# Kernel tuning notes

Hardware: AMD Instinct MI355X
Metric: run time of the kernel (lower is better)

The kernel has to match this reference:

```python
import jax, jax.numpy as jnp
import numpy as np

OUT_F, IN_F = 4096, 4096
WEIGHT_NUMEL = OUT_F * IN_F
NUM_CHUNKS, CHUNK_SIZE = 16384, 1024
D_ALPHA, HIDDEN = 64, 256
TOKENS = 256


def setup_inputs() -> dict:
    key = jax.random.key(0)
    ks = jax.random.split(key, 7)
    s = 0.05  # keep activations in a sane range
    return {
        "x": jax.random.normal(ks[0], (TOKENS, IN_F), jnp.float32),
        "codebook": jax.random.normal(ks[1], (NUM_CHUNKS, D_ALPHA), jnp.float32) * s,
        "w1": jax.random.normal(ks[2], (HIDDEN, D_ALPHA), jnp.float32) * s,
        "b1": jax.random.normal(ks[3], (HIDDEN,), jnp.float32) * s,
        "w2": jax.random.normal(ks[4], (CHUNK_SIZE, HIDDEN), jnp.float32) * s,
        "b2": jax.random.normal(ks[5], (CHUNK_SIZE,), jnp.float32) * s,
        "bias": jax.random.normal(ks[6], (OUT_F,), jnp.float32) * s,
    }


def reference(x, codebook, w1, b1, w2, b2, bias):
    # materialize_weight: alpha = codebook[start:start+num_chunks] (here: all rows)
    alpha = codebook[:NUM_CHUNKS]                                  # [num_chunks, d_alpha]
    # shared decoder psi: Linear -> GELU(exact) -> Linear (chunked loop == single GEMM)
    h = jax.nn.gelu(alpha @ w1.T + b1, approximate=False)          # [num_chunks, hidden]
    chunks = h @ w2.T + b2                                         # [num_chunks, chunk_size]
    w = chunks.reshape(-1)[:WEIGHT_NUMEL].reshape(OUT_F, IN_F)     # assemble weight
    # F.linear(x, w, b) = x @ w.T + b
    return x @ w.T + bias
```

## Files before the change

### kernel.cpp

```cpp
#include <hip/hip_runtime.h>
#include <math.h>

#define OUT_F      4096
#define IN_F       4096
#define NUM_CHUNKS 16384
#define CHUNK_SIZE 1024
#define D_ALPHA    64
#define HIDDEN     256
#define TOKENS     256

typedef __attribute__((ext_vector_type(8))) __bf16 bf16x8;
typedef __attribute__((ext_vector_type(4))) __bf16 bf16x4;
typedef __attribute__((ext_vector_type(4))) float f32x4;

__device__ __forceinline__ void gl2lds16(const void* g, void* l) {
    __builtin_amdgcn_global_load_lds(
        (const __attribute__((address_space(1))) void*)g,
        (__attribute__((address_space(3))) void*)l,
        16, 0, 0);
}

__global__ __launch_bounds__(256) void prep_kernel(
    const float* __restrict__ cb, const float* __restrict__ w1,
    const float* __restrict__ b1, const float* __restrict__ x,
    const float* __restrict__ b2, const float* __restrict__ w2,
    __bf16* __restrict__ H, __bf16* __restrict__ xb,
    float* __restrict__ xb2, __bf16* __restrict__ w2t) {
    __shared__ char smem[16384];
    const int b   = blockIdx.x;
    const int tid = threadIdx.x;

    if (b < 1024) {
        const int by = b >> 2;
        const int bx = b & 3;
        const int c0 = by * 64, h0 = bx * 64;
        __bf16* sA = (__bf16*)smem;
        __bf16* sB = (__bf16*)(smem + 8192);
        const float4* cb4 = reinterpret_cast<const float4*>(cb) + (size_t)by * 1024;
        const float4* w14 = reinterpret_cast<const float4*>(w1) + (size_t)bx * 1024;
#pragma unroll
        for (int q = 0; q < 4; ++q) {
            const int idx = q * 256 + tid;
            float4 va = cb4[idx];
            float4 vb = w14[idx];
            bf16x4 oa, ob;
            oa.x = (__bf16)va.x; oa.y = (__bf16)va.y; oa.z = (__bf16)va.z; oa.w = (__bf16)va.w;
            ob.x = (__bf16)vb.x; ob.y = (__bf16)vb.y; ob.z = (__bf16)vb.z; ob.w = (__bf16)vb.w;
            *reinterpret_cast<bf16x4*>(sA + idx * 4) = oa;
            *reinterpret_cast<bf16x4*>(sB + idx * 4) = ob;
        }
        __syncthreads();
        const int wave = tid >> 6, lane = tid & 63;
        const int wm = (wave & 1) * 32, wn = (wave >> 1) * 32;
        const int fr = lane & 15, fq = lane >> 4;
        f32x4 acc[2][2] = {};
        bf16x8 af[2][2], bv[2][2];
#pragma unroll
        for (int i = 0; i < 2; ++i)
#pragma unroll
            for (int u = 0; u < 2; ++u) {
                af[i][u] = *reinterpret_cast<const bf16x8*>(
                    sA + (wm + i * 16 + fr) * 64 + u * 32 + fq * 8);
                bv[i][u] = *reinterpret_cast<const bf16x8*>(
                    sB + (wn + i * 16 + fr) * 64 + u * 32 + fq * 8);
            }
#pragma unroll
        for (int u = 0; u < 2; ++u)
#pragma unroll
            for (int i = 0; i < 2; ++i)
#pragma unroll
                for (int j = 0; j < 2; ++j)
                    acc[i][j] = __builtin_amdgcn_mfma_f32_16x16x32_bf16(
                        af[i][u], bv[j][u], acc[i][j], 0, 0, 0);
#pragma unroll
        for (int j = 0; j < 2; ++j) {
            const int col = h0 + wn + j * 16 + fr;
            const float bb = b1[col];
#pragma unroll
            for (int i = 0; i < 2; ++i) {
                const int rbase = c0 + wm + i * 16 + fq * 4;
#pragma unroll
                for (int r = 0; r < 4; ++r) {
                    float v = acc[i][j][r] + bb;
                    float g = 0.5f * v * (1.0f + erff(v * 0.70710678118654752f));
                    H[(size_t)(rbase + r) * 256 + col] = (__bf16)g;
                }
            }
        }
    } else if (b < 1280) {
        float* ws_ = (float*)smem;
        const int t = b - 1024;
        const float4* xr  = reinterpret_cast<const float4*>(x + (size_t)t * IN_F);
        const float4* b24 = reinterpret_cast<const float4*>(b2);
        bf16x4* xb4 = reinterpret_cast<bf16x4*>(xb + (size_t)t * IN_F);
        float acc = 0.0f;
#pragma unroll
        for (int ii = 0; ii < 4; ++ii) {
            const int idx = ii * 256 + tid;
            float4 v = xr[idx];
            bf16x4 o;
            o.x = (__bf16)v.x; o.y = (__bf16)v.y; o.z = (__bf16)v.z; o.w = (__bf16)v.w;
            xb4[idx] = o;
            float4 bb = b24[idx & 255];
            acc += v.x * bb.x + v.y * bb.y + v.z * bb.z + v.w * bb.w;
        }
#pragma unroll
        for (int off = 32; off > 0; off >>= 1) acc += __shfl_down(acc, off, 64);
        if ((tid & 63) == 0) ws_[tid >> 6] = acc;
        __syncthreads();
        if (tid == 0) xb2[t] = ws_[0] + ws_[1] + ws_[2] + ws_[3];
    } else {
        float (*tile)[33] = (float (*)[33])smem;
        const int bb = b - 1280;
        const int h0 = (bb & 7) * 32;
        const int p0 = (bb >> 3) * 32;
        const int r = tid >> 5;
        const int c = tid & 31;
#pragma unroll
        for (int ii = 0; ii < 4; ++ii)
            tile[r + 8 * ii][c] = w2[(size_t)(p0 + r + 8 * ii) * HIDDEN + h0 + c];
        __syncthreads();
#pragma unroll
        for (int ii = 0; ii < 4; ++ii)
            w2t[(size_t)(h0 + r + 8 * ii) * CHUNK_SIZE + p0 + c] =
                (__bf16)tile[c][r + 8 * ii];
    }
}

template <int BK, int EPI>
__global__ __launch_bounds__(256) void gemm_bt64(
    const __bf16* __restrict__ A, const __bf16* __restrict__ B,
    const float* __restrict__ bias, const float* __restrict__ rowterm,
    void* __restrict__ Cv, int M, int N, int K) {
    __shared__ __bf16 sA[64 * BK];
    __shared__ __bf16 sB[64 * BK];
    const int tid = threadIdx.x;
    const int m0 = blockIdx.y * 64;
    const int n0 = blockIdx.x * 64;

    constexpr int NC = BK / 32;
    int rowc[NC], colc[NC];
#pragma unroll
    for (int c = 0; c < NC; ++c) {
        const int flat = c * 2048 + tid * 8;
        rowc[c] = flat / BK;
        colc[c] = flat % BK;
    }

    const int wave = tid >> 6, lane = tid & 63;
    const int wm = (wave & 1) * 32, wn = (wave >> 1) * 32;
    const int fr = lane & 15, fq = lane >> 4;

    f32x4 acc[2][2] = {};

    for (int k0 = 0; k0 < K; k0 += BK) {
#pragma unroll
        for (int c = 0; c < NC; ++c) {
            gl2lds16(A + (size_t)(m0 + rowc[c]) * K + k0 + colc[c],
                     sA + c * 2048 + tid * 8);
            gl2lds16(B + (size_t)(n0 + rowc[c]) * K + k0 + colc[c],
                     sB + c * 2048 + tid * 8);
        }
        __syncthreads();

#pragma unroll
        for (int u = 0; u < BK / 32; ++u) {
            bf16x8 af[2], bv[2];
#pragma unroll
            for (int i = 0; i < 2; ++i) {
                af[i] = *reinterpret_cast<const bf16x8*>(
                    sA + (wm + i * 16 + fr) * BK + u * 32 + fq * 8);
                bv[i] = *reinterpret_cast<const bf16x8*>(
                    sB + (wn + i * 16 + fr) * BK + u * 32 + fq * 8);
            }
#pragma unroll
            for (int i = 0; i < 2; ++i)
#pragma unroll
                for (int j = 0; j < 2; ++j)
                    acc[i][j] = __builtin_amdgcn_mfma_f32_16x16x32_bf16(
                        af[i], bv[j], acc[i][j], 0, 0, 0);
        }
        __syncthreads();
    }

    if (EPI == 0) {
        __bf16* C = (__bf16*)Cv;
#pragma unroll
        for (int j = 0; j < 2; ++j) {
            const int col = n0 + wn + j * 16 + fr;
#pragma unroll
            for (int i = 0; i < 2; ++i) {
                const int rbase = m0 + wm + i * 16 + fq * 4;
#pragma unroll
                for (int r = 0; r < 4; ++r)
                    C[(size_t)(rbase + r) * N + col] = (__bf16)acc[i][j][r];
            }
        }
    } else {
        float* C = (float*)Cv;
#pragma unroll
        for (int j = 0; j < 2; ++j) {
            const int col = n0 + wn + j * 16 + fr;
            const float bvs = bias[col];
#pragma unroll
            for (int i = 0; i < 2; ++i) {
                const int rbase = m0 + wm + i * 16 + fq * 4;
#pragma unroll
                for (int r = 0; r < 4; ++r)
                    C[(size_t)(rbase + r) * N + col] =
                        acc[i][j][r] + bvs + rowterm[rbase + r];
            }
        }
    }
}

extern "C" void kernel_launch(void* const* d_in, const int* in_sizes, int n_in,
                              void* d_out, int out_size, void* d_ws, size_t ws_size,
                              hipStream_t stream) {
    const float* x        = (const float*)d_in[0];
    const float* codebook = (const float*)d_in[1];
    const float* w1       = (const float*)d_in[2];
    const float* b1       = (const float*)d_in[3];
    const float* w2       = (const float*)d_in[4];
    const float* b2       = (const float*)d_in[5];
    const float* bias     = (const float*)d_in[6];
    float* out = (float*)d_out;

    char* ws = (char*)d_ws;
    __bf16* xb  = (__bf16*)(ws);
    __bf16* w2t = (__bf16*)(ws + (2u << 20));
    __bf16* H   = (__bf16*)(ws + (3u << 20));
    __bf16* Y   = (__bf16*)(ws + (11u << 20));
    float*  xb2 = (float*)(ws + (12u << 20));

    prep_kernel<<<1536, 256, 0, stream>>>(codebook, w1, b1, x, b2, w2,
                                          H, xb, xb2, w2t);

    {
        dim3 grid(HIDDEN / 64, 1024 / 64, 1);
        gemm_bt64<128, 0><<<grid, 256, 0, stream>>>(
            xb, w2t, nullptr, nullptr, Y, 1024, HIDDEN, 1024);
    }

    {
        dim3 grid(OUT_F / 64, TOKENS / 64, 1);
        gemm_bt64<128, 1><<<grid, 256, 0, stream>>>(
            Y, H, bias, xb2, out, TOKENS, OUT_F, 1024);
    }
}
```

Measured before the change: 106.3 us.

## Fuse x·W2 small GEMM into prep kernel, dropping separate launch and transposes

The x-by-W2 projection (Y) moves into new blocks of the prep kernel. Those blocks read fp32 x and w2 directly, convert to bf16 into LDS and transpose w2 on the fly. This removes one kernel launch and the intermediate xb and w2t buffers along with their global round-trips. The cost is a narrower 32x64 tile with a strided LDS transpose store, and the Y blocks now run alongside the H-generation blocks in one grid.

After: 103.7 us. 2.4% less time.

```diff
diff --git a/kernel.cpp b/kernel.cpp
--- a/kernel.cpp
+++ b/kernel.cpp
@@ -24,8 +24,8 @@
     const float* __restrict__ cb, const float* __restrict__ w1,
     const float* __restrict__ b1, const float* __restrict__ x,
     const float* __restrict__ b2, const float* __restrict__ w2,
-    __bf16* __restrict__ H, __bf16* __restrict__ xb,
-    float* __restrict__ xb2, __bf16* __restrict__ w2t) {
+    __bf16* __restrict__ H, __bf16* __restrict__ Y,
+    float* __restrict__ xb2) {
     __shared__ char smem[16384];
     const int b   = blockIdx.x;
     const int tid = threadIdx.x;
@@ -87,20 +87,72 @@
                 }
             }
         }
-    } else if (b < 1280) {
+    } else if (b < 1152) {
+        const int yb = b - 1024;
+        const int m0 = (yb >> 2) * 32;
+        const int n0 = (yb & 3) * 64;
+        __bf16* sA = (__bf16*)smem;
+        __bf16* sB = (__bf16*)(smem + 32 * 72 * 2);
+        const int wave = tid >> 6, lane = tid & 63;
+        const int fr = lane & 15, fq = lane >> 4;
+        const int wn = wave * 16;
+        const float4* xv  = reinterpret_cast<const float4*>(x);
+        const float4* w2v = reinterpret_cast<const float4*>(w2);
+        f32x4 acc[2] = {};
+
+        for (int k0 = 0; k0 < 1024; k0 += 64) {
+#pragma unroll
+            for (int q = 0; q < 2; ++q) {
+                const int idx = q * 256 + tid;
+                const int row = idx >> 4, c = idx & 15;
+                float4 v = xv[(size_t)(m0 + row) * 256 + (k0 >> 2) + c];
+                bf16x4 o;
+                o.x = (__bf16)v.x; o.y = (__bf16)v.y; o.z = (__bf16)v.z; o.w = (__bf16)v.w;
+                *reinterpret_cast<bf16x4*>(sA + row * 72 + c * 4) = o;
+            }
+#pragma unroll
+            for (int q = 0; q < 4; ++q) {
+                const int idx = q * 256 + tid;
+                const int kk = idx >> 4, c = idx & 15;
+                float4 v = w2v[(size_t)(k0 + kk) * 64 + (n0 >> 2) + c];
+                sB[(c * 4 + 0) * 72 + kk] = (__bf16)v.x;
+                sB[(c * 4 + 1) * 72 + kk] = (__bf16)v.y;
+                sB[(c * 4 + 2) * 72 + kk] = (__bf16)v.z;
+                sB[(c * 4 + 3) * 72 + kk] = (__bf16)v.w;
+            }
+            __syncthreads();
+#pragma unroll
+            for (int u = 0; u < 2; ++u) {
+                bf16x8 bv = *reinterpret_cast<const bf16x8*>(
+                    sB + (wn + fr) * 72 + u * 32 + fq * 8);
+#pragma unroll
+                for (int i = 0; i < 2; ++i) {
+                    bf16x8 af = *reinterpret_cast<const bf16x8*>(
+                        sA + (i * 16 + fr) * 72 + u * 32 + fq * 8);
+                    acc[i] = __builtin_amdgcn_mfma_f32_16x16x32_bf16(
+                        af, bv, acc[i], 0, 0, 0);
+                }
+            }
+            __syncthreads();
+        }
+#pragma unroll
+        for (int i = 0; i < 2; ++i) {
+            const int rbase = m0 + i * 16 + fq * 4;
+            const int col = n0 + wn + fr;
+#pragma unroll
+            for (int r = 0; r < 4; ++r)
+                Y[(size_t)(rbase + r) * 256 + col] = (__bf16)acc[i][r];
+        }
+    } else {
         float* ws_ = (float*)smem;
-        const int t = b - 1024;
+        const int t = b - 1152;
         const float4* xr  = reinterpret_cast<const float4*>(x + (size_t)t * IN_F);
         const float4* b24 = reinterpret_cast<const float4*>(b2);
-        bf16x4* xb4 = reinterpret_cast<bf16x4*>(xb + (size_t)t * IN_F);
         float acc = 0.0f;
 #pragma unroll
         for (int ii = 0; ii < 4; ++ii) {
             const int idx = ii * 256 + tid;
             float4 v = xr[idx];
-            bf16x4 o;
-            o.x = (__bf16)v.x; o.y = (__bf16)v.y; o.z = (__bf16)v.z; o.w = (__bf16)v.w;
-            xb4[idx] = o;
             float4 bb = b24[idx & 255];
             acc += v.x * bb.x + v.y * bb.y + v.z * bb.z + v.w * bb.w;
         }
@@ -109,29 +161,14 @@
         if ((tid & 63) == 0) ws_[tid >> 6] = acc;
         __syncthreads();
         if (tid == 0) xb2[t] = ws_[0] + ws_[1] + ws_[2] + ws_[3];
-    } else {
-        float (*tile)[33] = (float (*)[33])smem;
-        const int bb = b - 1280;
-        const int h0 = (bb & 7) * 32;
-        const int p0 = (bb >> 3) * 32;
-        const int r = tid >> 5;
-        const int c = tid & 31;
-#pragma unroll
-        for (int ii = 0; ii < 4; ++ii)
-            tile[r + 8 * ii][c] = w2[(size_t)(p0 + r + 8 * ii) * HIDDEN + h0 + c];
-        __syncthreads();
-#pragma unroll
-        for (int ii = 0; ii < 4; ++ii)
-            w2t[(size_t)(h0 + r + 8 * ii) * CHUNK_SIZE + p0 + c] =
-                (__bf16)tile[c][r + 8 * ii];
-    }
-}
-
-template <int BK, int EPI>
+    }
+}
+
+template <int BK>
 __global__ __launch_bounds__(256) void gemm_bt64(
     const __bf16* __restrict__ A, const __bf16* __restrict__ B,
     const float* __restrict__ bias, const float* __restrict__ rowterm,
-    void* __restrict__ Cv, int M, int N, int K) {
+    float* __restrict__ C, int M, int N, int K) {
     __shared__ __bf16 sA[64 * BK];
     __shared__ __bf16 sB[64 * BK];
     const int tid = threadIdx.x;
@@ -183,33 +220,17 @@
         __syncthreads();
     }
 
-    if (EPI == 0) {
-        __bf16* C = (__bf16*)Cv;
-#pragma unroll
-        for (int j = 0; j < 2; ++j) {
-            const int col = n0 + wn + j * 16 + fr;
-#pragma unroll
-            for (int i = 0; i < 2; ++i) {
-                const int rbase = m0 + wm + i * 16 + fq * 4;
-#pragma unroll
-                for (int r = 0; r < 4; ++r)
-                    C[(size_t)(rbase + r) * N + col] = (__bf16)acc[i][j][r];
-            }
-        }
-    } else {
-        float* C = (float*)Cv;
-#pragma unroll
-        for (int j = 0; j < 2; ++j) {
-            const int col = n0 + wn + j * 16 + fr;
-            const float bvs = bias[col];
-#pragma unroll
-            for (int i = 0; i < 2; ++i) {
-                const int rbase = m0 + wm + i * 16 + fq * 4;
-#pragma unroll
-                for (int r = 0; r < 4; ++r)
-                    C[(size_t)(rbase + r) * N + col] =
-                        acc[i][j][r] + bvs + rowterm[rbase + r];
-            }
+#pragma unroll
+    for (int j = 0; j < 2; ++j) {
+        const int col = n0 + wn + j * 16 + fr;
+        const float bvs = bias[col];
+#pragma unroll
+        for (int i = 0; i < 2; ++i) {
+            const int rbase = m0 + wm + i * 16 + fq * 4;
+#pragma unroll
+            for (int r = 0; r < 4; ++r)
+                C[(size_t)(rbase + r) * N + col] =
+                    acc[i][j][r] + bvs + rowterm[rbase + r];
         }
     }
 }
@@ -227,24 +248,16 @@
     float* out = (float*)d_out;
 
     char* ws = (char*)d_ws;
-    __bf16* xb  = (__bf16*)(ws);
-    __bf16* w2t = (__bf16*)(ws + (2u << 20));
-    __bf16* H   = (__bf16*)(ws + (3u << 20));
-    __bf16* Y   = (__bf16*)(ws + (11u << 20));
-    float*  xb2 = (float*)(ws + (12u << 20));
-
-    prep_kernel<<<1536, 256, 0, stream>>>(codebook, w1, b1, x, b2, w2,
-                                          H, xb, xb2, w2t);
-
-    {
-        dim3 grid(HIDDEN / 64, 1024 / 64, 1);
-        gemm_bt64<128, 0><<<grid, 256, 0, stream>>>(
-            xb, w2t, nullptr, nullptr, Y, 1024, HIDDEN, 1024);
-    }
+    __bf16* H   = (__bf16*)(ws);
+    __bf16* Y   = (__bf16*)(ws + (8u << 20));
+    float*  xb2 = (float*)(ws + (8u << 20) + (512u << 10));
+
+    prep_kernel<<<1408, 256, 0, stream>>>(codebook, w1, b1, x, b2, w2,
+                                          H, Y, xb2);
 
     {
         dim3 grid(OUT_F / 64, TOKENS / 64, 1);
-        gemm_bt64<128, 1><<<grid, 256, 0, stream>>>(
+        gemm_bt64<128><<<grid, 256, 0, stream>>>(
             Y, H, bias, xb2, out, TOKENS, OUT_F, 1024);
     }
 }
```
